# Kernel tuning notes

Measured on AMD Instinct MI355X. Metric: run time of the kernel, lower is better.

## Reference

```python
import jax, jax.numpy as jnp
import numpy as np

N, E = 100000, 600000
IN, HID, OUT, ED = 128, 128, 64, 32


def _gine_conv(x, src, dst, edge_feats, We, be, Wa, ba, Wb, bb):
    # GINEConv: msg = relu(x_j + Linear(edge_attr)); out = MLP((1+eps)*x + sum msg), eps=0
    e = edge_feats @ We + be                      # [E, C]
    msg = jax.nn.relu(x[src] + e)                 # gather + edge-add
    agg = jax.ops.segment_sum(msg, dst, num_segments=x.shape[0])
    h = x + agg                                   # eps = 0
    return jax.nn.relu(h @ Wa + ba) @ Wb + bb     # 2-layer MLP


def setup_inputs() -> dict:
    key = jax.random.key(0)
    ks = jax.random.split(key, 20)
    g = lambda k, shp, fan: jax.random.normal(k, shp, jnp.float32) * (1.0 / np.sqrt(fan))
    return {
        "x": jax.random.normal(ks[0], (N, IN), jnp.float32),
        "edge_index": jax.random.randint(ks[1], (2, E), 0, N, dtype=jnp.int32),
        "edge_feats": jax.random.normal(ks[2], (E, ED), jnp.float32),
        # conv1: edge lin (ED->IN), nn1 (IN->HID->HID)
        "We1": g(ks[3], (ED, IN), ED), "be1": jnp.zeros((IN,), jnp.float32),
        "W1a": g(ks[4], (IN, HID), IN), "b1a": jnp.zeros((HID,), jnp.float32),
        "W1b": g(ks[5], (HID, HID), HID), "b1b": jnp.zeros((HID,), jnp.float32),
        # conv2: edge lin (ED->HID), nn2 (HID->HID->HID)
        "We2": g(ks[6], (ED, HID), ED), "be2": jnp.zeros((HID,), jnp.float32),
        "W2a": g(ks[7], (HID, HID), HID), "b2a": jnp.zeros((HID,), jnp.float32),
        "W2b": g(ks[8], (HID, HID), HID), "b2b": jnp.zeros((HID,), jnp.float32),
        # heads
        "Wfc1": g(ks[9], (HID, HID), HID), "bfc1": jnp.zeros((HID,), jnp.float32),
        "Wfc2": g(ks[10], (HID, OUT), HID), "bfc2": jnp.zeros((OUT,), jnp.float32),
    }


def reference(x, edge_index, edge_feats,
              We1, be1, W1a, b1a, W1b, b1b,
              We2, be2, W2a, b2a, W2b, b2b,
              Wfc1, bfc1, Wfc2, bfc2):
    src, dst = edge_index[0], edge_index[1]  # source_to_target flow
    h = _gine_conv(x, src, dst, edge_feats, We1, be1, W1a, b1a, W1b, b1b)
    h = jnp.tanh(h)                          # dropout: eval-mode identity
    h = _gine_conv(h, src, dst, edge_feats, We2, be2, W2a, b2a, W2b, b2b)
    h = jnp.tanh(h)
    h = jnp.tanh(h @ Wfc1 + bfc1)
    return h @ Wfc2 + bfc2
```

## Files before the change

### kernel.cpp

```cpp
#include <hip/hip_runtime.h>
#include <hip/hip_fp16.h>
#include <math.h>

#define N_NODES 100000
#define N_EDGES 600000
#define NB_SCAN ((N_NODES + 1023) / 1024)

typedef unsigned short u16;
typedef __bf16 bf16x8 __attribute__((ext_vector_type(8)));
typedef float  f32x4  __attribute__((ext_vector_type(4)));

__device__ __forceinline__ u16 f2bf(float f) {
    union { float f; unsigned u; } c; c.f = f;
    unsigned u = c.u + 0x7fffu + ((c.u >> 16) & 1u);
    return (u16)(u >> 16);
}
__device__ __forceinline__ float bf2f(u16 h) {
    union { unsigned u; float f; } c; c.u = ((unsigned)h) << 16;
    return c.f;
}
__device__ __forceinline__ float fast_tanh(float x) {
    float e = __expf(2.0f * x);
    return 1.0f - 2.0f * __builtin_amdgcn_rcpf(e + 1.0f);
}

__global__ void hist_k(const int* __restrict__ dst, int* __restrict__ counts,
                       int* __restrict__ rank)
{
    int e = blockIdx.x * 256 + threadIdx.x;
    if (e < N_EDGES) rank[e] = atomicAdd(&counts[dst[e]], 1);
}

__global__ void scan_a_k(const int* __restrict__ counts, int* __restrict__ row_ptr,
                         int* __restrict__ blockSums)
{
    __shared__ int s[256];
    const int t = threadIdx.x;
    const int base = blockIdx.x * 1024 + t * 4;
    int c[4];
#pragma unroll
    for (int j = 0; j < 4; ++j) c[j] = (base + j < N_NODES) ? counts[base + j] : 0;
    const int tot = c[0] + c[1] + c[2] + c[3];
    s[t] = tot;
    __syncthreads();
    for (int off = 1; off < 256; off <<= 1) {
        int v = (t >= off) ? s[t - off] : 0;
        __syncthreads();
        s[t] += v;
        __syncthreads();
    }
    int run = s[t] - tot;
#pragma unroll
    for (int j = 0; j < 4; ++j) {
        if (base + j < N_NODES) row_ptr[base + j] = run;
        run += c[j];
    }
    if (t == 255) blockSums[blockIdx.x] = s[255];
}

__global__ void scan_b_k(const int* __restrict__ blockSums, int* __restrict__ blockOffs)
{
    if (threadIdx.x == 0) {
        int run = 0;
        for (int b = 0; b < NB_SCAN; ++b) { blockOffs[b] = run; run += blockSums[b]; }
    }
}

__global__ void scan_c_k(int* __restrict__ row_ptr, const int* __restrict__ blockOffs)
{
    int i = blockIdx.x * 256 + threadIdx.x;
    if (i < N_NODES) row_ptr[i] += blockOffs[i >> 10];
    if (i == 0) row_ptr[N_NODES] = N_EDGES;
}

__global__ void scatter_k(const int* __restrict__ src, const int* __restrict__ dst,
                          const int* __restrict__ row_ptr, const int* __restrict__ rank,
                          int* __restrict__ perm, int* __restrict__ src_sorted,
                          int* __restrict__ dst_sorted)
{
    int e = blockIdx.x * 256 + threadIdx.x;
    if (e < N_EDGES) {
        int pos = row_ptr[dst[e]] + rank[e];
        perm[pos] = e;
        src_sorted[pos] = src[e];
        dst_sorted[pos] = dst[e];
    }
}

__global__ void wprep_k(const float* __restrict__ W1a, const float* __restrict__ W1b,
                        const float* __restrict__ W2a, const float* __restrict__ W2b,
                        const float* __restrict__ Wf1, const float* __restrict__ Wf2,
                        u16* __restrict__ wT)
{
    int idx = blockIdx.x * 256 + threadIdx.x;
    if (idx >= 90112) return;
    int m, local;
    if      (idx < 16384) { m = 0; local = idx; }
    else if (idx < 32768) { m = 1; local = idx - 16384; }
    else if (idx < 49152) { m = 2; local = idx - 32768; }
    else if (idx < 65536) { m = 3; local = idx - 49152; }
    else if (idx < 81920) { m = 4; local = idx - 65536; }
    else                  { m = 5; local = idx - 81920; }
    const int N = (m == 5) ? 64 : 128;
    const float* src = (m == 0) ? W1a : (m == 1) ? W1b : (m == 2) ? W2a
                     : (m == 3) ? W2b : (m == 4) ? Wf1 : Wf2;
    const int k = local / N, n = local % N;
    const float w = src[k * N + n];
    const u16 hi = f2bf(w);
    const u16 lo = f2bf(w - bf2f(hi));
    const int base = m * 32768;
    const int sz   = (m == 5) ? 8192 : 16384;
    wT[base + n * 128 + k]      = hi;
    wT[base + sz + n * 128 + k] = lo;
}

__global__ __launch_bounds__(256) void fused_conv_k(
    const float* __restrict__ x, const float* __restrict__ ef,
    const int* __restrict__ perm, const int* __restrict__ src_s,
    const int* __restrict__ dst_s, const int* __restrict__ row_ptr,
    const float* __restrict__ We, const float* __restrict__ be,
    float* __restrict__ agg)
{
    __shared__ __align__(16) char smem[33792];
    float (*sWe)[128] = (float (*)[128])smem;
    float (*sEf)[36]  = (float (*)[36])(smem + 16384);
    float (*msg)[132] = (float (*)[132])smem;
    __shared__ int sSrc[64];
    __shared__ int sDst[64];

    const int t  = threadIdx.x;
    const int i0 = blockIdx.x * 64;

    {
        const float4* W4 = (const float4*)We;
        float4* S4 = (float4*)(&sWe[0][0]);
#pragma unroll
        for (int j = 0; j < 4; ++j) S4[t + j * 256] = W4[t + j * 256];
    }
    if (t < 64) { sSrc[t] = src_s[i0 + t]; sDst[t] = dst_s[i0 + t]; }
    {
        const int row = t >> 2;
        const int q   = t & 3;
        const int e   = perm[i0 + row];
        const float4* p = (const float4*)(ef + (size_t)e * 32);
        const float4 v0 = p[q];
        const float4 v1 = p[q + 4];
        *(float4*)(&sEf[row][q * 4])       = v0;
        *(float4*)(&sEf[row][(q + 4) * 4]) = v1;
    }
    __syncthreads();

    const int c  = (t & 31) * 4;
    const int s0 = (t >> 5) * 8;
    float4 acc[8];
    const float4 bv = *(const float4*)(be + c);
#pragma unroll
    for (int s = 0; s < 8; ++s) acc[s] = bv;

#pragma unroll 8
    for (int k = 0; k < 32; ++k) {
        const float4 w = *(const float4*)(&sWe[k][c]);
#pragma unroll
        for (int s = 0; s < 8; ++s) {
            const float a = sEf[s0 + s][k];
            acc[s].x = fmaf(a, w.x, acc[s].x);
            acc[s].y = fmaf(a, w.y, acc[s].y);
            acc[s].z = fmaf(a, w.z, acc[s].z);
            acc[s].w = fmaf(a, w.w, acc[s].w);
        }
    }

#pragma unroll
    for (int s = 0; s < 8; ++s) {
        const float4 xv = *(const float4*)(x + (size_t)sSrc[s0 + s] * 128 + c);
        acc[s].x = fmaxf(acc[s].x + xv.x, 0.f);
        acc[s].y = fmaxf(acc[s].y + xv.y, 0.f);
        acc[s].z = fmaxf(acc[s].z + xv.z, 0.f);
        acc[s].w = fmaxf(acc[s].w + xv.w, 0.f);
    }
    __syncthreads();
#pragma unroll
    for (int s = 0; s < 8; ++s) *(float4*)(&msg[s0 + s][c]) = acc[s];
    __syncthreads();

    const int lane = t & 63, wave = t >> 6;
    const int c2 = lane * 2;
    const int nF = sDst[0], nL = sDst[63];
    for (int n = nF + wave; n <= nL; n += 4) {
        const int rs = row_ptr[n];
        const int re = row_ptr[n + 1];
        const int lo = rs > i0 ? rs : i0;
        const int hi = re < i0 + 64 ? re : i0 + 64;
        float a0 = 0.f, a1 = 0.f;
        for (int i = lo; i < hi; ++i) {
            const float2 v = *(const float2*)(&msg[i - i0][c2]);
            a0 += v.x; a1 += v.y;
        }
        float* dp = agg + (size_t)n * 128 + c2;
        const bool interior = (rs >= i0) && (re <= i0 + 64);
        if (interior) {
            *(float2*)dp = make_float2(a0, a1);
        } else if (hi > lo) {
            atomicAdd(dp,     a0);
            atomicAdd(dp + 1, a1);
        }
    }
}

template <int NT2, bool TANH1, bool TANHF, bool ADDAGG>
__global__ __launch_bounds__(256, 4) void mlp2_mfma_k(
    const float* __restrict__ xin, const float* __restrict__ agg,
    const u16* __restrict__ WaT_hi, const u16* __restrict__ WaT_lo,
    const float* __restrict__ ba,
    const u16* __restrict__ WbT_hi, const u16* __restrict__ WbT_lo,
    const float* __restrict__ bb,
    float* __restrict__ out)
{
    __shared__ u16 sHi[64][136];
    __shared__ u16 sLo[64][136];
    const int tid = threadIdx.x;
    const int n0  = blockIdx.x * 64;

    {
        const int mrow = tid >> 5, kq = tid & 31;
#pragma unroll
        for (int g = 0; g < 8; ++g) {
            const int row  = g * 8 + mrow;
            const int node = n0 + row;
            float4 v = make_float4(0.f, 0.f, 0.f, 0.f);
            if (node < N_NODES) {
                v = *(const float4*)(xin + (size_t)node * 128 + kq * 4);
                if (ADDAGG) {
                    float4 a4 = *(const float4*)(agg + (size_t)node * 128 + kq * 4);
                    v.x += a4.x; v.y += a4.y; v.z += a4.z; v.w += a4.w;
                }
            }
            const u16 h0 = f2bf(v.x), h1 = f2bf(v.y), h2 = f2bf(v.z), h3 = f2bf(v.w);
            const u16 l0 = f2bf(v.x - bf2f(h0)), l1 = f2bf(v.y - bf2f(h1));
            const u16 l2 = f2bf(v.z - bf2f(h2)), l3 = f2bf(v.w - bf2f(h3));
            *(uint2*)&sHi[row][kq * 4] =
                make_uint2((unsigned)h0 | ((unsigned)h1 << 16), (unsigned)h2 | ((unsigned)h3 << 16));
            *(uint2*)&sLo[row][kq * 4] =
                make_uint2((unsigned)l0 | ((unsigned)l1 << 16), (unsigned)l2 | ((unsigned)l3 << 16));
        }
    }
    __syncthreads();

    const int lane = tid & 63, wave = tid >> 6;
    const int quad = lane >> 4, col = lane & 15;

    f32x4 accA[2][4];
#pragma unroll
    for (int j = 0; j < 2; ++j) {
        const int nt = wave * 2 + j;
        const float bv = ba[nt * 16 + col];
#pragma unroll
        for (int m = 0; m < 4; ++m) accA[j][m] = (f32x4){bv, bv, bv, bv};

        bf16x8 bHi[4], bLo[4];
#pragma unroll
        for (int k0 = 0; k0 < 4; ++k0) {
            const size_t off = (size_t)(nt * 16 + col) * 128 + k0 * 32 + quad * 8;
            bHi[k0] = *(const bf16x8*)(WaT_hi + off);
            bLo[k0] = *(const bf16x8*)(WaT_lo + off);
        }
#pragma unroll 2
        for (int m = 0; m < 4; ++m) {
#pragma unroll
            for (int k0 = 0; k0 < 4; ++k0) {
                const bf16x8 aHi = *(const bf16x8*)&sHi[m * 16 + col][k0 * 32 + quad * 8];
                const bf16x8 aLo = *(const bf16x8*)&sLo[m * 16 + col][k0 * 32 + quad * 8];
                accA[j][m] = __builtin_amdgcn_mfma_f32_16x16x32_bf16(aHi, bHi[k0], accA[j][m], 0, 0, 0);
                accA[j][m] = __builtin_amdgcn_mfma_f32_16x16x32_bf16(aHi, bLo[k0], accA[j][m], 0, 0, 0);
                accA[j][m] = __builtin_amdgcn_mfma_f32_16x16x32_bf16(aLo, bHi[k0], accA[j][m], 0, 0, 0);
            }
        }
    }
    __syncthreads();

#pragma unroll
    for (int j = 0; j < 2; ++j) {
        const int ct = (wave * 2 + j) * 16 + col;
#pragma unroll
        for (int m = 0; m < 4; ++m) {
#pragma unroll
            for (int r = 0; r < 4; ++r) {
                float v = TANH1 ? fast_tanh(accA[j][m][r]) : fmaxf(accA[j][m][r], 0.f);
                const u16 hv = f2bf(v);
                const u16 lv = f2bf(v - bf2f(hv));
                const int row = m * 16 + quad * 4 + r;
                sHi[row][ct] = hv;
                sLo[row][ct] = lv;
            }
        }
    }
    __syncthreads();

    constexpr int JB   = NT2 / 4;
    constexpr int NOUT = NT2 * 16;
#pragma unroll
    for (int j = 0; j < JB; ++j) {
        const int nt = wave * JB + j;
        const float bv = bb[nt * 16 + col];
        f32x4 accB[4];
#pragma unroll
        for (int m = 0; m < 4; ++m) accB[m] = (f32x4){bv, bv, bv, bv};

        bf16x8 bHi[4], bLo[4];
#pragma unroll
        for (int k0 = 0; k0 < 4; ++k0) {
            const size_t off = (size_t)(nt * 16 + col) * 128 + k0 * 32 + quad * 8;
            bHi[k0] = *(const bf16x8*)(WbT_hi + off);
            bLo[k0] = *(const bf16x8*)(WbT_lo + off);
        }
#pragma unroll 2
        for (int m = 0; m < 4; ++m) {
#pragma unroll
            for (int k0 = 0; k0 < 4; ++k0) {
                const bf16x8 tHi = *(const bf16x8*)&sHi[m * 16 + col][k0 * 32 + quad * 8];
                const bf16x8 tLo = *(const bf16x8*)&sLo[m * 16 + col][k0 * 32 + quad * 8];
                accB[m] = __builtin_amdgcn_mfma_f32_16x16x32_bf16(tHi, bHi[k0], accB[m], 0, 0, 0);
                accB[m] = __builtin_amdgcn_mfma_f32_16x16x32_bf16(tHi, bLo[k0], accB[m], 0, 0, 0);
                accB[m] = __builtin_amdgcn_mfma_f32_16x16x32_bf16(tLo, bHi[k0], accB[m], 0, 0, 0);
            }
        }
#pragma unroll
        for (int m = 0; m < 4; ++m) {
#pragma unroll
            for (int r = 0; r < 4; ++r) {
                const int node = n0 + m * 16 + quad * 4 + r;
                if (node < N_NODES) {
                    float v = accB[m][r];
                    if (TANHF) v = fast_tanh(v);
                    out[(size_t)node * NOUT + nt * 16 + col] = v;
                }
            }
        }
    }
}

extern "C" void kernel_launch(void* const* d_in, const int* in_sizes, int n_in,
                              void* d_out, int out_size, void* d_ws, size_t ws_size,
                              hipStream_t stream)
{
    const float* x   = (const float*)d_in[0];
    const int*   ei  = (const int*)  d_in[1];
    const float* ef  = (const float*)d_in[2];
    const float* We1 = (const float*)d_in[3];
    const float* be1 = (const float*)d_in[4];
    const float* W1a = (const float*)d_in[5];
    const float* b1a = (const float*)d_in[6];
    const float* W1b = (const float*)d_in[7];
    const float* b1b = (const float*)d_in[8];
    const float* We2 = (const float*)d_in[9];
    const float* be2 = (const float*)d_in[10];
    const float* W2a = (const float*)d_in[11];
    const float* b2a = (const float*)d_in[12];
    const float* W2b = (const float*)d_in[13];
    const float* b2b = (const float*)d_in[14];
    const float* Wf1 = (const float*)d_in[15];
    const float* bf1 = (const float*)d_in[16];
    const float* Wf2 = (const float*)d_in[17];
    const float* bf2 = (const float*)d_in[18];
    float* out = (float*)d_out;

    const int* src = ei;
    const int* dst = ei + N_EDGES;

    float*  agg     = (float*)d_ws;
    float*  h       = agg + (size_t)N_NODES * 128;
    int*    row_ptr = (int*)(h + (size_t)N_NODES * 128);
    int*    perm    = row_ptr + (N_NODES + 8);
    int*    src_s   = perm + N_EDGES;
    int*    dst_srt = src_s + N_EDGES;
    u16*    wT      = (u16*)(dst_srt + N_EDGES);
    int* counts    = (int*)agg;
    int* rank      = counts + N_NODES;
    int* blockSums = rank + N_EDGES;
    int* blockOffs = blockSums + NB_SCAN;

    u16* W1aT = wT;
    u16* W1bT = wT + 32768;
    u16* W2aT = wT + 65536;
    u16* W2bT = wT + 98304;
    u16* Wf1T = wT + 131072;
    u16* Wf2T = wT + 163840;

    const int mlpGrid = (N_NODES + 63) / 64;
    const int eGrid   = (N_EDGES + 255) / 256;
    const int nGrid   = (N_NODES + 255) / 256;
    const int fcGrid  = N_EDGES / 64;
    const int wpGrid  = (90112 + 255) / 256;

    hipMemsetAsync(counts, 0, (size_t)N_NODES * sizeof(int), stream);
    hist_k   <<<eGrid,   256, 0, stream>>>(dst, counts, rank);
    wprep_k  <<<wpGrid,  256, 0, stream>>>(W1a, W1b, W2a, W2b, Wf1, Wf2, wT);
    scan_a_k <<<NB_SCAN, 256, 0, stream>>>(counts, row_ptr, blockSums);
    scan_b_k <<<1,        64, 0, stream>>>(blockSums, blockOffs);
    scan_c_k <<<nGrid,   256, 0, stream>>>(row_ptr, blockOffs);
    scatter_k<<<eGrid,   256, 0, stream>>>(src, dst, row_ptr, rank, perm, src_s, dst_srt);

    hipMemsetAsync(agg, 0, (size_t)N_NODES * 128 * sizeof(float), stream);
    fused_conv_k<<<fcGrid, 256, 0, stream>>>(x, ef, perm, src_s, dst_srt, row_ptr,
                                             We1, be1, agg);
    mlp2_mfma_k<8, false, true, true><<<mlpGrid, 256, 0, stream>>>(
        x, agg, W1aT, W1aT + 16384, b1a, W1bT, W1bT + 16384, b1b, h);

    hipMemsetAsync(agg, 0, (size_t)N_NODES * 128 * sizeof(float), stream);
    fused_conv_k<<<fcGrid, 256, 0, stream>>>(h, ef, perm, src_s, dst_srt, row_ptr,
                                             We2, be2, agg);
    mlp2_mfma_k<8, false, true, true><<<mlpGrid, 256, 0, stream>>>(
        h, agg, W2aT, W2aT + 16384, b2a, W2bT, W2bT + 16384, b2b, h);

    mlp2_mfma_k<4, true, false, false><<<mlpGrid, 256, 0, stream>>>(
        h, nullptr, Wf1T, Wf1T + 16384, bf1, Wf2T, Wf2T + 8192, bf2, out);
}
```

Measured before the change: 573.8 us.

## Compute edge linear in fused conv with split-bf16 MFMA instead of scalar FMA

Replaces the per-edge 32x128 edge-feature linear layer in the fused conv kernel with bf16 MFMA 16x16x32 instructions. Precision is kept near fp32 by splitting both operands into hi/lo parts and summing three products. The edge weights are pre-transposed and split in the weight-prep kernel, and edge features are converted to hi/lo bf16 in shared memory. This drops the 16KB shared weight staging and adds a launch_bounds occupancy hint. The x gather now uses per-column scalar loads instead of float4, which may cost some memory efficiency.

```diff
diff --git a/kernel.cpp b/kernel.cpp
--- a/kernel.cpp
+++ b/kernel.cpp
@@ -90,10 +90,25 @@
 __global__ void wprep_k(const float* __restrict__ W1a, const float* __restrict__ W1b,
                         const float* __restrict__ W2a, const float* __restrict__ W2b,
                         const float* __restrict__ Wf1, const float* __restrict__ Wf2,
+                        const float* __restrict__ We1, const float* __restrict__ We2,
                         u16* __restrict__ wT)
 {
     int idx = blockIdx.x * 256 + threadIdx.x;
-    if (idx >= 90112) return;
+    if (idx >= 98304) return;
+    if (idx >= 90112) {
+        int l = idx - 90112;
+        const int m = l >> 12;
+        l &= 4095;
+        const float* src = m ? We2 : We1;
+        const int k = l >> 7, n = l & 127;
+        const float w = src[k * 128 + n];
+        const u16 hi = f2bf(w);
+        const u16 lo = f2bf(w - bf2f(hi));
+        const int base = 180224 + m * 8192;
+        wT[base + n * 32 + k]        = hi;
+        wT[base + 4096 + n * 32 + k] = lo;
+        return;
+    }
     int m, local;
     if      (idx < 16384) { m = 0; local = idx; }
     else if (idx < 32768) { m = 1; local = idx - 16384; }
@@ -114,16 +129,16 @@
     wT[base + sz + n * 128 + k] = lo;
 }
 
-__global__ __launch_bounds__(256) void fused_conv_k(
+__global__ __launch_bounds__(256, 4) void fused_conv_k(
     const float* __restrict__ x, const float* __restrict__ ef,
     const int* __restrict__ perm, const int* __restrict__ src_s,
     const int* __restrict__ dst_s, const int* __restrict__ row_ptr,
-    const float* __restrict__ We, const float* __restrict__ be,
-    float* __restrict__ agg)
+    const u16* __restrict__ WeT_hi, const u16* __restrict__ WeT_lo,
+    const float* __restrict__ be, float* __restrict__ agg)
 {
     __shared__ __align__(16) char smem[33792];
-    float (*sWe)[128] = (float (*)[128])smem;
-    float (*sEf)[36]  = (float (*)[36])(smem + 16384);
+    u16 (*efHi)[40]   = (u16 (*)[40])smem;
+    u16 (*efLo)[40]   = (u16 (*)[40])(smem + 5120);
     float (*msg)[132] = (float (*)[132])smem;
     __shared__ int sSrc[64];
     __shared__ int sDst[64];
@@ -131,59 +146,89 @@
     const int t  = threadIdx.x;
     const int i0 = blockIdx.x * 64;
 
-    {
-        const float4* W4 = (const float4*)We;
-        float4* S4 = (float4*)(&sWe[0][0]);
-#pragma unroll
-        for (int j = 0; j < 4; ++j) S4[t + j * 256] = W4[t + j * 256];
-    }
     if (t < 64) { sSrc[t] = src_s[i0 + t]; sDst[t] = dst_s[i0 + t]; }
     {
         const int row = t >> 2;
         const int q   = t & 3;
         const int e   = perm[i0 + row];
-        const float4* p = (const float4*)(ef + (size_t)e * 32);
-        const float4 v0 = p[q];
-        const float4 v1 = p[q + 4];
-        *(float4*)(&sEf[row][q * 4])       = v0;
-        *(float4*)(&sEf[row][(q + 4) * 4]) = v1;
-    }
-    __syncthreads();
-
-    const int c  = (t & 31) * 4;
-    const int s0 = (t >> 5) * 8;
-    float4 acc[8];
-    const float4 bv = *(const float4*)(be + c);
-#pragma unroll
-    for (int s = 0; s < 8; ++s) acc[s] = bv;
-
-#pragma unroll 8
-    for (int k = 0; k < 32; ++k) {
-        const float4 w = *(const float4*)(&sWe[k][c]);
-#pragma unroll
-        for (int s = 0; s < 8; ++s) {
-            const float a = sEf[s0 + s][k];
-            acc[s].x = fmaf(a, w.x, acc[s].x);
-            acc[s].y = fmaf(a, w.y, acc[s].y);
-            acc[s].z = fmaf(a, w.z, acc[s].z);
-            acc[s].w = fmaf(a, w.w, acc[s].w);
-        }
-    }
-
-#pragma unroll
-    for (int s = 0; s < 8; ++s) {
-        const float4 xv = *(const float4*)(x + (size_t)sSrc[s0 + s] * 128 + c);
-        acc[s].x = fmaxf(acc[s].x + xv.x, 0.f);
-        acc[s].y = fmaxf(acc[s].y + xv.y, 0.f);
-        acc[s].z = fmaxf(acc[s].z + xv.z, 0.f);
-        acc[s].w = fmaxf(acc[s].w + xv.w, 0.f);
-    }
-    __syncthreads();
-#pragma unroll
-    for (int s = 0; s < 8; ++s) *(float4*)(&msg[s0 + s][c]) = acc[s];
+        const float* p = ef + (size_t)e * 32 + q * 8;
+        const float4 v0 = *(const float4*)(p);
+        const float4 v1 = *(const float4*)(p + 4);
+        const float vv[8] = {v0.x, v0.y, v0.z, v0.w, v1.x, v1.y, v1.z, v1.w};
+        unsigned hp[4], lp[4];
+#pragma unroll
+        for (int i = 0; i < 4; ++i) {
+            const u16 h0 = f2bf(vv[2 * i]),     h1 = f2bf(vv[2 * i + 1]);
+            const u16 l0 = f2bf(vv[2 * i]     - bf2f(h0));
+            const u16 l1 = f2bf(vv[2 * i + 1] - bf2f(h1));
+            hp[i] = (unsigned)h0 | ((unsigned)h1 << 16);
+            lp[i] = (unsigned)l0 | ((unsigned)l1 << 16);
+        }
+        *(uint4*)&efHi[row][q * 8] = make_uint4(hp[0], hp[1], hp[2], hp[3]);
+        *(uint4*)&efLo[row][q * 8] = make_uint4(lp[0], lp[1], lp[2], lp[3]);
+    }
     __syncthreads();
 
     const int lane = t & 63, wave = t >> 6;
+    const int quad = lane >> 4, col = lane & 15;
+
+    bf16x8 bHi[2], bLo[2];
+#pragma unroll
+    for (int j = 0; j < 2; ++j) {
+        const int nt = wave * 2 + j;
+        const size_t off = (size_t)(nt * 16 + col) * 32 + quad * 8;
+        bHi[j] = *(const bf16x8*)(WeT_hi + off);
+        bLo[j] = *(const bf16x8*)(WeT_lo + off);
+    }
+
+    float xv[2][4][4];
+#pragma unroll
+    for (int m = 0; m < 4; ++m)
+#pragma unroll
+        for (int r = 0; r < 4; ++r) {
+            const int s = sSrc[m * 16 + quad * 4 + r];
+            const float* xp = x + (size_t)s * 128 + wave * 32 + col;
+            xv[0][m][r] = xp[0];
+            xv[1][m][r] = xp[16];
+        }
+
+    f32x4 acc[2][4];
+#pragma unroll
+    for (int j = 0; j < 2; ++j) {
+        const float bv = be[wave * 32 + j * 16 + col];
+#pragma unroll
+        for (int m = 0; m < 4; ++m) acc[j][m] = (f32x4){bv, bv, bv, bv};
+    }
+#pragma unroll
+    for (int m = 0; m < 4; ++m) {
+        const bf16x8 aHi = *(const bf16x8*)&efHi[m * 16 + col][quad * 8];
+        const bf16x8 aLo = *(const bf16x8*)&efLo[m * 16 + col][quad * 8];
+#pragma unroll
+        for (int j = 0; j < 2; ++j) {
+            acc[j][m] = __builtin_amdgcn_mfma_f32_16x16x32_bf16(aHi, bHi[j], acc[j][m], 0, 0, 0);
+            acc[j][m] = __builtin_amdgcn_mfma_f32_16x16x32_bf16(aHi, bLo[j], acc[j][m], 0, 0, 0);
+            acc[j][m] = __builtin_amdgcn_mfma_f32_16x16x32_bf16(aLo, bHi[j], acc[j][m], 0, 0, 0);
+        }
+    }
+
+#pragma unroll
+    for (int j = 0; j < 2; ++j)
+#pragma unroll
+        for (int m = 0; m < 4; ++m)
+#pragma unroll
+            for (int r = 0; r < 4; ++r)
+                acc[j][m][r] = fmaxf(acc[j][m][r] + xv[j][m][r], 0.f);
+
+    __syncthreads();
+#pragma unroll
+    for (int j = 0; j < 2; ++j)
+#pragma unroll
+        for (int m = 0; m < 4; ++m)
+#pragma unroll
+            for (int r = 0; r < 4; ++r)
+                msg[m * 16 + quad * 4 + r][wave * 32 + j * 16 + col] = acc[j][m][r];
+    __syncthreads();
+
     const int c2 = lane * 2;
     const int nF = sDst[0], nL = sDst[63];
     for (int n = nF + wave; n <= nL; n += 4) {
@@ -385,16 +430,18 @@
     u16* W2bT = wT + 98304;
     u16* Wf1T = wT + 131072;
     u16* Wf2T = wT + 163840;
+    u16* We1T = wT + 180224;
+    u16* We2T = wT + 188416;
 
     const int mlpGrid = (N_NODES + 63) / 64;
     const int eGrid   = (N_EDGES + 255) / 256;
     const int nGrid   = (N_NODES + 255) / 256;
     const int fcGrid  = N_EDGES / 64;
-    const int wpGrid  = (90112 + 255) / 256;
+    const int wpGrid  = (98304 + 255) / 256;
 
     hipMemsetAsync(counts, 0, (size_t)N_NODES * sizeof(int), stream);
     hist_k   <<<eGrid,   256, 0, stream>>>(dst, counts, rank);
-    wprep_k  <<<wpGrid,  256, 0, stream>>>(W1a, W1b, W2a, W2b, Wf1, Wf2, wT);
+    wprep_k  <<<wpGrid,  256, 0, stream>>>(W1a, W1b, W2a, W2b, Wf1, Wf2, We1, We2, wT);
     scan_a_k <<<NB_SCAN, 256, 0, stream>>>(counts, row_ptr, blockSums);
     scan_b_k <<<1,        64, 0, stream>>>(blockSums, blockOffs);
     scan_c_k <<<nGrid,   256, 0, stream>>>(row_ptr, blockOffs);
@@ -402,13 +449,13 @@
 
     hipMemsetAsync(agg, 0, (size_t)N_NODES * 128 * sizeof(float), stream);
     fused_conv_k<<<fcGrid, 256, 0, stream>>>(x, ef, perm, src_s, dst_srt, row_ptr,
-                                             We1, be1, agg);
+                                             We1T, We1T + 4096, be1, agg);
     mlp2_mfma_k<8, false, true, true><<<mlpGrid, 256, 0, stream>>>(
         x, agg, W1aT, W1aT + 16384, b1a, W1bT, W1bT + 16384, b1b, h);
 
     hipMemsetAsync(agg, 0, (size_t)N_NODES * 128 * sizeof(float), stream);
     fused_conv_k<<<fcGrid, 256, 0, stream>>>(h, ef, perm, src_s, dst_srt, row_ptr,
-                                             We2, be2, agg);
+                                             We2T, We2T + 4096, be2, agg);
     mlp2_mfma_k<8, false, true, true><<<mlpGrid, 256, 0, stream>>>(
         h, agg, W2aT, W2aT + 16384, b2a, W2bT, W2bT + 16384, b2b, h);
 
```

After: 550.2 us. 1.04x faster.
